# Optimization experiments

Measured on AMD Instinct MI355X. Metric: run time of the kernel, lower is better.

## Reference

```python
import jax, jax.numpy as jnp
import numpy as np

EPS = 1e-9

def setup_inputs() -> dict:
    key = jax.random.key(0)
    k1, k2 = jax.random.split(key)
    B, N, D, E = 4, 4096, 2048, 64
    x = jax.random.normal(k1, (B, N, D), dtype=jnp.float32)
    w_gating = jax.random.normal(k2, (E, D), dtype=jnp.float32) * (1.0 / np.sqrt(D))
    return {"x": x, "w_gating": w_gating}

def reference(x, w_gating):
    # logits: [B, N, E] = x @ W^T  (nn.Linear, no bias)
    logits = jnp.einsum("bnd,ed->bne", x, w_gating)
    probs = jax.nn.softmax(logits, axis=-1)
    # top-2 selection; equivalent to argmax -> scatter(-inf) -> argmax chain
    top2_vals, top2_idx = jax.lax.top_k(probs, 2)  # [B, N, 2]
    denom = top2_vals[..., 0] + top2_vals[..., 1] + EPS
    combine_weights = top2_vals / denom[..., None]  # [B, N, 2]
    expert_index = top2_idx.astype(jnp.int32)       # [B, N, 2]
    return combine_weights, expert_index
```

## Files before the change

### kernel.cpp

```cpp
#include <hip/hip_runtime.h>
#include <math.h>

#define K_DIM 2048
#define E_DIM 64
#define BM 32
#define NW 8
#define KW (K_DIM / NW)
#define KS 32
#define NSTEP (KW / KS)
#define WSCALE 64.0f
#define RSTRIDE (E_DIM + 4)

typedef _Float16 f16x8 __attribute__((ext_vector_type(8)));
typedef float    f32x4 __attribute__((ext_vector_type(4)));

__global__ void pack_w_kernel(const float* __restrict__ w, _Float16* __restrict__ wpk) {
    int tid  = (int)blockIdx.x * 256 + (int)threadIdx.x;
    int lane = tid & 63;
    int n    = (tid >> 6) & 3;
    int kk   = tid >> 8;
    int col  = n * 16 + (lane & 15);
    int k    = kk * 32 + (lane >> 4) * 8;
    const float* src = w + (size_t)col * K_DIM + k;
    _Float16* hi = wpk + (size_t)tid * 8;
    _Float16* lo = hi + (size_t)K_DIM * E_DIM;
    #pragma unroll
    for (int j = 0; j < 8; ++j) {
        float v = src[j] * WSCALE;
        _Float16 h = (_Float16)v;
        hi[j] = h;
        lo[j] = (_Float16)(v - (float)h);
    }
}

__global__ __launch_bounds__(512, 4) void mfma_gate_kernel(
    const float* __restrict__ x,
    const _Float16* __restrict__ wpk,
    float* __restrict__ out, int M)
{
    __shared__ float red[4][BM][RSTRIDE];

    const int t    = (int)threadIdx.x;
    const int lane = t & 63;
    const int wave = __builtin_amdgcn_readfirstlane(t >> 6);
    const int lr   = lane & 15;
    const int ks   = lane >> 4;
    const int rowbase = (int)blockIdx.x * BM;
    const size_t k0 = (size_t)wave * KW;

    f32x4 acc[2][4];
    #pragma unroll
    for (int m = 0; m < 2; ++m)
        #pragma unroll
        for (int n = 0; n < 4; ++n)
            acc[m][n] = (f32x4){0.f, 0.f, 0.f, 0.f};

    const float* xa0 = x + (size_t)(rowbase + lr) * K_DIM + k0 + (size_t)ks * 8;
    const float* xa1 = xa0 + (size_t)16 * K_DIM;
    const _Float16* wph = wpk + ((size_t)(wave * NSTEP) * 4 * 64 + lane) * 8;
    const _Float16* wpl = wph + (size_t)K_DIM * E_DIM;

    float4 c00 = *(const float4*)(xa0);
    float4 c01 = *(const float4*)(xa0 + 4);
    float4 c10 = *(const float4*)(xa1);
    float4 c11 = *(const float4*)(xa1 + 4);

    #pragma unroll 2
    for (int s = 0; s < NSTEP; ++s) {
        const int sn = (s + 1) & (NSTEP - 1);
        float4 n00 = *(const float4*)(xa0 + sn * KS);
        float4 n01 = *(const float4*)(xa0 + sn * KS + 4);
        float4 n10 = *(const float4*)(xa1 + sn * KS);
        float4 n11 = *(const float4*)(xa1 + sn * KS + 4);

        f16x8 bh[4], bl[4];
        #pragma unroll
        for (int n = 0; n < 4; ++n) {
            bh[n] = *(const f16x8*)(wph + ((size_t)s * 4 + n) * 512);
            bl[n] = *(const f16x8*)(wpl + ((size_t)s * 4 + n) * 512);
        }

        f16x8 ah[2], al[2];
        {
            float u0[8] = {c00.x, c00.y, c00.z, c00.w, c01.x, c01.y, c01.z, c01.w};
            float u1[8] = {c10.x, c10.y, c10.z, c10.w, c11.x, c11.y, c11.z, c11.w};
            #pragma unroll
            for (int j = 0; j < 8; ++j) {
                _Float16 h0 = (_Float16)u0[j];
                ah[0][j] = h0;
                al[0][j] = (_Float16)(u0[j] - (float)h0);
                _Float16 h1 = (_Float16)u1[j];
                ah[1][j] = h1;
                al[1][j] = (_Float16)(u1[j] - (float)h1);
            }
        }

        #pragma unroll
        for (int m = 0; m < 2; ++m)
            #pragma unroll
            for (int n = 0; n < 4; ++n) {
                acc[m][n] = __builtin_amdgcn_mfma_f32_16x16x32_f16(ah[m], bh[n], acc[m][n], 0, 0, 0);
                acc[m][n] = __builtin_amdgcn_mfma_f32_16x16x32_f16(ah[m], bl[n], acc[m][n], 0, 0, 0);
                acc[m][n] = __builtin_amdgcn_mfma_f32_16x16x32_f16(al[m], bh[n], acc[m][n], 0, 0, 0);
            }

        c00 = n00; c01 = n01; c10 = n10; c11 = n11;
    }

    const float inv = 1.0f / WSCALE;
    if (wave >= 4) {
        #pragma unroll
        for (int m = 0; m < 2; ++m)
            #pragma unroll
            for (int n = 0; n < 4; ++n)
                #pragma unroll
                for (int j = 0; j < 4; ++j)
                    red[wave - 4][m * 16 + ks * 4 + j][n * 16 + lr] = acc[m][n][j] * inv;
    }
    __syncthreads();
    if (wave < 4) {
        #pragma unroll
        for (int m = 0; m < 2; ++m)
            #pragma unroll
            for (int n = 0; n < 4; ++n)
                #pragma unroll
                for (int j = 0; j < 4; ++j)
                    red[wave][m * 16 + ks * 4 + j][n * 16 + lr] += acc[m][n][j] * inv;
    }
    __syncthreads();

    #pragma unroll 1
    for (int rr = 0; rr < BM / NW; ++rr) {
        const int r = wave * (BM / NW) + rr;
        float l = red[0][r][lane] + red[1][r][lane] + red[2][r][lane] + red[3][r][lane];

        float m = l;
        #pragma unroll
        for (int off = 32; off >= 1; off >>= 1)
            m = fmaxf(m, __shfl_xor(m, off));

        float e = expf(l - m);
        float z = e;
        #pragma unroll
        for (int off = 32; off >= 1; off >>= 1)
            z += __shfl_xor(z, off);
        const float p = e / z;

        float v1 = p; int i1 = lane;
        #pragma unroll
        for (int off = 32; off >= 1; off >>= 1) {
            float ov = __shfl_xor(v1, off);
            int   oi = __shfl_xor(i1, off);
            if (ov > v1 || (ov == v1 && oi < i1)) { v1 = ov; i1 = oi; }
        }

        float v2 = (lane == i1) ? -1.0f : p; int i2 = lane;
        #pragma unroll
        for (int off = 32; off >= 1; off >>= 1) {
            float ov = __shfl_xor(v2, off);
            int   oi = __shfl_xor(i2, off);
            if (ov > v2 || (ov == v2 && oi < i2)) { v2 = ov; i2 = oi; }
        }

        if (lane == 0) {
            const size_t row = (size_t)rowbase + r;
            const float denom = v1 + v2 + 1e-9f;
            out[row * 2 + 0] = v1 / denom;
            out[row * 2 + 1] = v2 / denom;
            out[(size_t)M * 2 + row * 2 + 0] = (float)i1;
            out[(size_t)M * 2 + row * 2 + 1] = (float)i2;
        }
    }
}

__global__ __launch_bounds__(512, 2) void mfma_gate_kernel_raw(
    const float* __restrict__ x,
    const float* __restrict__ w,
    float* __restrict__ out, int M)
{
    __shared__ float red[4][BM][RSTRIDE];
    const int t    = (int)threadIdx.x;
    const int lane = t & 63;
    const int wave = __builtin_amdgcn_readfirstlane(t >> 6);
    const int lr   = lane & 15;
    const int ks   = lane >> 4;
    const int rowbase = (int)blockIdx.x * BM;
    const size_t k0 = (size_t)wave * KW;

    f32x4 acc[2][4];
    #pragma unroll
    for (int m = 0; m < 2; ++m)
        #pragma unroll
        for (int n = 0; n < 4; ++n)
            acc[m][n] = (f32x4){0.f, 0.f, 0.f, 0.f};

    const float* xa0 = x + (size_t)(rowbase + lr) * K_DIM + k0 + (size_t)ks * 8;
    const float* xa1 = xa0 + (size_t)16 * K_DIM;

    for (int s = 0; s < NSTEP; ++s) {
        f16x8 ah[2], al[2];
        #pragma unroll
        for (int m = 0; m < 2; ++m) {
            const float* p = (m == 0 ? xa0 : xa1) + (size_t)s * KS;
            float4 u0 = *(const float4*)p;
            float4 u1 = *(const float4*)(p + 4);
            float uu[8] = {u0.x, u0.y, u0.z, u0.w, u1.x, u1.y, u1.z, u1.w};
            #pragma unroll
            for (int j = 0; j < 8; ++j) {
                _Float16 h = (_Float16)uu[j];
                ah[m][j] = h;
                al[m][j] = (_Float16)(uu[j] - (float)h);
            }
        }
        f16x8 bh[4], bl[4];
        #pragma unroll
        for (int n = 0; n < 4; ++n) {
            const float* p = w + (size_t)(n * 16 + lr) * K_DIM + k0 + (size_t)s * KS + (size_t)ks * 8;
            float4 u0 = *(const float4*)p;
            float4 u1 = *(const float4*)(p + 4);
            float uu[8] = {u0.x, u0.y, u0.z, u0.w, u1.x, u1.y, u1.z, u1.w};
            #pragma unroll
            for (int j = 0; j < 8; ++j) {
                float v = uu[j] * WSCALE;
                _Float16 h = (_Float16)v;
                bh[n][j] = h;
                bl[n][j] = (_Float16)(v - (float)h);
            }
        }
        #pragma unroll
        for (int m = 0; m < 2; ++m)
            #pragma unroll
            for (int n = 0; n < 4; ++n) {
                acc[m][n] = __builtin_amdgcn_mfma_f32_16x16x32_f16(ah[m], bh[n], acc[m][n], 0, 0, 0);
                acc[m][n] = __builtin_amdgcn_mfma_f32_16x16x32_f16(ah[m], bl[n], acc[m][n], 0, 0, 0);
                acc[m][n] = __builtin_amdgcn_mfma_f32_16x16x32_f16(al[m], bh[n], acc[m][n], 0, 0, 0);
            }
    }

    const float inv = 1.0f / WSCALE;
    if (wave >= 4) {
        #pragma unroll
        for (int m = 0; m < 2; ++m)
            #pragma unroll
            for (int n = 0; n < 4; ++n)
                #pragma unroll
                for (int j = 0; j < 4; ++j)
                    red[wave - 4][m * 16 + ks * 4 + j][n * 16 + lr] = acc[m][n][j] * inv;
    }
    __syncthreads();
    if (wave < 4) {
        #pragma unroll
        for (int m = 0; m < 2; ++m)
            #pragma unroll
            for (int n = 0; n < 4; ++n)
                #pragma unroll
                for (int j = 0; j < 4; ++j)
                    red[wave][m * 16 + ks * 4 + j][n * 16 + lr] += acc[m][n][j] * inv;
    }
    __syncthreads();

    #pragma unroll 1
    for (int rr = 0; rr < BM / NW; ++rr) {
        const int r = wave * (BM / NW) + rr;
        float l = red[0][r][lane] + red[1][r][lane] + red[2][r][lane] + red[3][r][lane];
        float m = l;
        #pragma unroll
        for (int off = 32; off >= 1; off >>= 1)
            m = fmaxf(m, __shfl_xor(m, off));
        float e = expf(l - m);
        float z = e;
        #pragma unroll
        for (int off = 32; off >= 1; off >>= 1)
            z += __shfl_xor(z, off);
        const float p = e / z;
        float v1 = p; int i1 = lane;
        #pragma unroll
        for (int off = 32; off >= 1; off >>= 1) {
            float ov = __shfl_xor(v1, off);
            int   oi = __shfl_xor(i1, off);
            if (ov > v1 || (ov == v1 && oi < i1)) { v1 = ov; i1 = oi; }
        }
        float v2 = (lane == i1) ? -1.0f : p; int i2 = lane;
        #pragma unroll
        for (int off = 32; off >= 1; off >>= 1) {
            float ov = __shfl_xor(v2, off);
            int   oi = __shfl_xor(i2, off);
            if (ov > v2 || (ov == v2 && oi < i2)) { v2 = ov; i2 = oi; }
        }
        if (lane == 0) {
            const size_t row = (size_t)rowbase + r;
            const float denom = v1 + v2 + 1e-9f;
            out[row * 2 + 0] = v1 / denom;
            out[row * 2 + 1] = v2 / denom;
            out[(size_t)M * 2 + row * 2 + 0] = (float)i1;
            out[(size_t)M * 2 + row * 2 + 1] = (float)i2;
        }
    }
}

extern "C" void kernel_launch(void* const* d_in, const int* in_sizes, int n_in,
                              void* d_out, int out_size, void* d_ws, size_t ws_size,
                              hipStream_t stream)
{
    const float* x = (const float*)d_in[0];
    const float* w = (const float*)d_in[1];
    float* out = (float*)d_out;
    const int M = in_sizes[0] / K_DIM;
    const int grid = M / BM;

    const size_t pack_bytes = (size_t)K_DIM * E_DIM * 2 * sizeof(_Float16);
    if (ws_size >= pack_bytes) {
        pack_w_kernel<<<64, 256, 0, stream>>>(w, (_Float16*)d_ws);
        mfma_gate_kernel<<<grid, 512, 0, stream>>>(x, (const _Float16*)d_ws, out, M);
    } else {
        mfma_gate_kernel_raw<<<grid, 512, 0, stream>>>(x, w, out, M);
    }
}
```

Before: 51.54 us.

## Stage x tiles through LDS with async global_load_lds and split experts across waves

The main kernel now uses 4 waves, each owning 16 experts across the full K dimension, instead of 8 waves splitting K. It double-buffers 32x128 x tiles into LDS with swizzled direct global-to-LDS loads. This removes the cross-wave K reduction through shared memory, and all waves share each x tile instead of every wave loading its own K slice into registers. In exchange it adds a barrier per chunk and halves the threads per block, which may reduce latency hiding. The raw fallback is adjusted to 256 threads with a single-pass reduction.

```diff
diff --git a/kernel.cpp b/kernel.cpp
--- a/kernel.cpp
+++ b/kernel.cpp
@@ -4,15 +4,21 @@
 #define K_DIM 2048
 #define E_DIM 64
 #define BM 32
-#define NW 8
-#define KW (K_DIM / NW)
-#define KS 32
-#define NSTEP (KW / KS)
+#define NW 4
+#define KC 128
+#define NT (K_DIM / KC)
 #define WSCALE 64.0f
-#define RSTRIDE (E_DIM + 4)
+#define LGSTRIDE 68
 
 typedef _Float16 f16x8 __attribute__((ext_vector_type(8)));
 typedef float    f32x4 __attribute__((ext_vector_type(4)));
+
+__device__ __forceinline__ void load_lds16(const float* g, float* l) {
+    __builtin_amdgcn_global_load_lds(
+        (const __attribute__((address_space(1))) unsigned int*)(g),
+        (__attribute__((address_space(3))) unsigned int*)(l),
+        16, 0, 0);
+}
 
 __global__ void pack_w_kernel(const float* __restrict__ w, _Float16* __restrict__ wpk) {
     int tid  = (int)blockIdx.x * 256 + (int)threadIdx.x;
@@ -33,12 +39,12 @@
     }
 }
 
-__global__ __launch_bounds__(512, 4) void mfma_gate_kernel(
+__global__ __launch_bounds__(256, 2) void mfma_gate_kernel(
     const float* __restrict__ x,
     const _Float16* __restrict__ wpk,
     float* __restrict__ out, int M)
 {
-    __shared__ float red[4][BM][RSTRIDE];
+    __shared__ float stg[2][BM * KC];
 
     const int t    = (int)threadIdx.x;
     const int lane = t & 63;
@@ -46,93 +52,86 @@
     const int lr   = lane & 15;
     const int ks   = lane >> 4;
     const int rowbase = (int)blockIdx.x * BM;
-    const size_t k0 = (size_t)wave * KW;
-
-    f32x4 acc[2][4];
+
+    f32x4 acc[2];
+    acc[0] = (f32x4){0.f, 0.f, 0.f, 0.f};
+    acc[1] = (f32x4){0.f, 0.f, 0.f, 0.f};
+
+    const float* gsrc[4];
+    #pragma unroll
+    for (int j = 0; j < 4; ++j) {
+        const int slot = wave * 4 + j;
+        const int row  = slot * 2 + (lane >> 5);
+        const int c4   = (lane & 31) ^ (row & 7);
+        gsrc[j] = x + (size_t)(rowbase + row) * K_DIM + c4 * 4;
+    }
+
+    const _Float16* wph = wpk + (size_t)wave * 512 + (size_t)lane * 8;
+    const _Float16* wpl = wph + (size_t)K_DIM * E_DIM;
+
+    #pragma unroll
+    for (int j = 0; j < 4; ++j)
+        load_lds16(gsrc[j], &stg[0][(wave * 4 + j) * 256]);
+    __syncthreads();
+
+    #pragma unroll 1
+    for (int c = 0; c < NT; ++c) {
+        const int cur = c & 1;
+
+        f16x8 bh[4], bl[4];
+        #pragma unroll
+        for (int s2 = 0; s2 < 4; ++s2) {
+            const size_t off = (size_t)((c * 4 + s2) * 4) * 512;
+            bh[s2] = *(const f16x8*)(wph + off);
+            bl[s2] = *(const f16x8*)(wpl + off);
+        }
+
+        if (c + 1 < NT) {
+            #pragma unroll
+            for (int j = 0; j < 4; ++j)
+                load_lds16(gsrc[j] + (size_t)(c + 1) * KC,
+                           &stg[cur ^ 1][(wave * 4 + j) * 256]);
+        }
+
+        const float* bufc = stg[cur];
+        const int key = lr & 7;
+        #pragma unroll
+        for (int s2 = 0; s2 < 4; ++s2) {
+            #pragma unroll
+            for (int m = 0; m < 2; ++m) {
+                const int row = m * 16 + lr;
+                const int c4a = s2 * 8 + ks * 2;
+                float4 a0 = *(const float4*)&bufc[row * KC + ((c4a)     ^ key) * 4];
+                float4 a1 = *(const float4*)&bufc[row * KC + ((c4a + 1) ^ key) * 4];
+                float u[8] = {a0.x, a0.y, a0.z, a0.w, a1.x, a1.y, a1.z, a1.w};
+                f16x8 ah, al;
+                #pragma unroll
+                for (int j = 0; j < 8; ++j) {
+                    _Float16 h = (_Float16)u[j];
+                    ah[j] = h;
+                    al[j] = (_Float16)(u[j] - (float)h);
+                }
+                acc[m] = __builtin_amdgcn_mfma_f32_16x16x32_f16(ah, bh[s2], acc[m], 0, 0, 0);
+                acc[m] = __builtin_amdgcn_mfma_f32_16x16x32_f16(ah, bl[s2], acc[m], 0, 0, 0);
+                acc[m] = __builtin_amdgcn_mfma_f32_16x16x32_f16(al, bh[s2], acc[m], 0, 0, 0);
+            }
+        }
+        __syncthreads();
+    }
+
+    float* lg = &stg[0][0];
+    const float inv = 1.0f / WSCALE;
     #pragma unroll
     for (int m = 0; m < 2; ++m)
         #pragma unroll
-        for (int n = 0; n < 4; ++n)
-            acc[m][n] = (f32x4){0.f, 0.f, 0.f, 0.f};
-
-    const float* xa0 = x + (size_t)(rowbase + lr) * K_DIM + k0 + (size_t)ks * 8;
-    const float* xa1 = xa0 + (size_t)16 * K_DIM;
-    const _Float16* wph = wpk + ((size_t)(wave * NSTEP) * 4 * 64 + lane) * 8;
-    const _Float16* wpl = wph + (size_t)K_DIM * E_DIM;
-
-    float4 c00 = *(const float4*)(xa0);
-    float4 c01 = *(const float4*)(xa0 + 4);
-    float4 c10 = *(const float4*)(xa1);
-    float4 c11 = *(const float4*)(xa1 + 4);
-
-    #pragma unroll 2
-    for (int s = 0; s < NSTEP; ++s) {
-        const int sn = (s + 1) & (NSTEP - 1);
-        float4 n00 = *(const float4*)(xa0 + sn * KS);
-        float4 n01 = *(const float4*)(xa0 + sn * KS + 4);
-        float4 n10 = *(const float4*)(xa1 + sn * KS);
-        float4 n11 = *(const float4*)(xa1 + sn * KS + 4);
-
-        f16x8 bh[4], bl[4];
-        #pragma unroll
-        for (int n = 0; n < 4; ++n) {
-            bh[n] = *(const f16x8*)(wph + ((size_t)s * 4 + n) * 512);
-            bl[n] = *(const f16x8*)(wpl + ((size_t)s * 4 + n) * 512);
-        }
-
-        f16x8 ah[2], al[2];
-        {
-            float u0[8] = {c00.x, c00.y, c00.z, c00.w, c01.x, c01.y, c01.z, c01.w};
-            float u1[8] = {c10.x, c10.y, c10.z, c10.w, c11.x, c11.y, c11.z, c11.w};
-            #pragma unroll
-            for (int j = 0; j < 8; ++j) {
-                _Float16 h0 = (_Float16)u0[j];
-                ah[0][j] = h0;
-                al[0][j] = (_Float16)(u0[j] - (float)h0);
-                _Float16 h1 = (_Float16)u1[j];
-                ah[1][j] = h1;
-                al[1][j] = (_Float16)(u1[j] - (float)h1);
-            }
-        }
-
-        #pragma unroll
-        for (int m = 0; m < 2; ++m)
-            #pragma unroll
-            for (int n = 0; n < 4; ++n) {
-                acc[m][n] = __builtin_amdgcn_mfma_f32_16x16x32_f16(ah[m], bh[n], acc[m][n], 0, 0, 0);
-                acc[m][n] = __builtin_amdgcn_mfma_f32_16x16x32_f16(ah[m], bl[n], acc[m][n], 0, 0, 0);
-                acc[m][n] = __builtin_amdgcn_mfma_f32_16x16x32_f16(al[m], bh[n], acc[m][n], 0, 0, 0);
-            }
-
-        c00 = n00; c01 = n01; c10 = n10; c11 = n11;
-    }
-
-    const float inv = 1.0f / WSCALE;
-    if (wave >= 4) {
-        #pragma unroll
-        for (int m = 0; m < 2; ++m)
-            #pragma unroll
-            for (int n = 0; n < 4; ++n)
-                #pragma unroll
-                for (int j = 0; j < 4; ++j)
-                    red[wave - 4][m * 16 + ks * 4 + j][n * 16 + lr] = acc[m][n][j] * inv;
-    }
-    __syncthreads();
-    if (wave < 4) {
-        #pragma unroll
-        for (int m = 0; m < 2; ++m)
-            #pragma unroll
-            for (int n = 0; n < 4; ++n)
-                #pragma unroll
-                for (int j = 0; j < 4; ++j)
-                    red[wave][m * 16 + ks * 4 + j][n * 16 + lr] += acc[m][n][j] * inv;
-    }
+        for (int j = 0; j < 4; ++j)
+            lg[(m * 16 + ks * 4 + j) * LGSTRIDE + wave * 16 + lr] = acc[m][j] * inv;
     __syncthreads();
 
     #pragma unroll 1
     for (int rr = 0; rr < BM / NW; ++rr) {
         const int r = wave * (BM / NW) + rr;
-        float l = red[0][r][lane] + red[1][r][lane] + red[2][r][lane] + red[3][r][lane];
+        float l = lg[r * LGSTRIDE + lane];
 
         float m = l;
         #pragma unroll
@@ -173,19 +172,19 @@
     }
 }
 
-__global__ __launch_bounds__(512, 2) void mfma_gate_kernel_raw(
+__global__ __launch_bounds__(256, 2) void mfma_gate_kernel_raw(
     const float* __restrict__ x,
     const float* __restrict__ w,
     float* __restrict__ out, int M)
 {
-    __shared__ float red[4][BM][RSTRIDE];
+    __shared__ float red[4][BM][LGSTRIDE];
     const int t    = (int)threadIdx.x;
     const int lane = t & 63;
     const int wave = __builtin_amdgcn_readfirstlane(t >> 6);
     const int lr   = lane & 15;
     const int ks   = lane >> 4;
     const int rowbase = (int)blockIdx.x * BM;
-    const size_t k0 = (size_t)wave * KW;
+    const size_t k0 = (size_t)wave * 512;
 
     f32x4 acc[2][4];
     #pragma unroll
@@ -197,11 +196,11 @@
     const float* xa0 = x + (size_t)(rowbase + lr) * K_DIM + k0 + (size_t)ks * 8;
     const float* xa1 = xa0 + (size_t)16 * K_DIM;
 
-    for (int s = 0; s < NSTEP; ++s) {
+    for (int s = 0; s < 16; ++s) {
         f16x8 ah[2], al[2];
         #pragma unroll
         for (int m = 0; m < 2; ++m) {
-            const float* p = (m == 0 ? xa0 : xa1) + (size_t)s * KS;
+            const float* p = (m == 0 ? xa0 : xa1) + (size_t)s * 32;
             float4 u0 = *(const float4*)p;
             float4 u1 = *(const float4*)(p + 4);
             float uu[8] = {u0.x, u0.y, u0.z, u0.w, u1.x, u1.y, u1.z, u1.w};
@@ -215,7 +214,7 @@
         f16x8 bh[4], bl[4];
         #pragma unroll
         for (int n = 0; n < 4; ++n) {
-            const float* p = w + (size_t)(n * 16 + lr) * K_DIM + k0 + (size_t)s * KS + (size_t)ks * 8;
+            const float* p = w + (size_t)(n * 16 + lr) * K_DIM + k0 + (size_t)s * 32 + (size_t)ks * 8;
             float4 u0 = *(const float4*)p;
             float4 u1 = *(const float4*)(p + 4);
             float uu[8] = {u0.x, u0.y, u0.z, u0.w, u1.x, u1.y, u1.z, u1.w};
@@ -238,30 +237,18 @@
     }
 
     const float inv = 1.0f / WSCALE;
-    if (wave >= 4) {
-        #pragma unroll
-        for (int m = 0; m < 2; ++m)
-            #pragma unroll
-            for (int n = 0; n < 4; ++n)
-                #pragma unroll
-                for (int j = 0; j < 4; ++j)
-                    red[wave - 4][m * 16 + ks * 4 + j][n * 16 + lr] = acc[m][n][j] * inv;
-    }
+    #pragma unroll
+    for (int m = 0; m < 2; ++m)
+        #pragma unroll
+        for (int n = 0; n < 4; ++n)
+            #pragma unroll
+            for (int j = 0; j < 4; ++j)
+                red[wave][m * 16 + ks * 4 + j][n * 16 + lr] = acc[m][n][j] * inv;
     __syncthreads();
-    if (wave < 4) {
-        #pragma unroll
-        for (int m = 0; m < 2; ++m)
-            #pragma unroll
-            for (int n = 0; n < 4; ++n)
-                #pragma unroll
-                for (int j = 0; j < 4; ++j)
-                    red[wave][m * 16 + ks * 4 + j][n * 16 + lr] += acc[m][n][j] * inv;
-    }
-    __syncthreads();
 
     #pragma unroll 1
-    for (int rr = 0; rr < BM / NW; ++rr) {
-        const int r = wave * (BM / NW) + rr;
+    for (int rr = 0; rr < BM / 4; ++rr) {
+        const int r = wave * (BM / 4) + rr;
         float l = red[0][r][lane] + red[1][r][lane] + red[2][r][lane] + red[3][r][lane];
         float m = l;
         #pragma unroll
@@ -311,8 +298,8 @@
     const size_t pack_bytes = (size_t)K_DIM * E_DIM * 2 * sizeof(_Float16);
     if (ws_size >= pack_bytes) {
         pack_w_kernel<<<64, 256, 0, stream>>>(w, (_Float16*)d_ws);
-        mfma_gate_kernel<<<grid, 512, 0, stream>>>(x, (const _Float16*)d_ws, out, M);
+        mfma_gate_kernel<<<grid, 256, 0, stream>>>(x, (const _Float16*)d_ws, out, M);
     } else {
-        mfma_gate_kernel_raw<<<grid, 512, 0, stream>>>(x, w, out, M);
-    }
-}
+        mfma_gate_kernel_raw<<<grid, 256, 0, stream>>>(x, w, out, M);
+    }
+}
```

Measured after the change: 62.38 us. +21.0%, slower.
